# Kernel optimization log

Hardware: AMD Instinct MI355X
Metric: run time of the kernel (lower is better)

Reference implementation:

```python
import jax, jax.numpy as jnp
import numpy as np

HEAD = 8  # number of attention heads (init kwarg)


def setup_inputs() -> dict:
    key = jax.random.key(0)
    k1, k2, k3 = jax.random.split(key, 3)
    b, H, W, c = 8, 32, 32, 512
    dim = 512
    x = jax.random.normal(k1, (b, H, W, c), dtype=jnp.float32)
    # 1x1 Conv == per-pixel matmul over channels
    w_qkv = jax.random.normal(k2, (c, 3 * dim), dtype=jnp.float32) * (c ** -0.5)
    w_out = jax.random.normal(k3, (dim, dim), dtype=jnp.float32) * (dim ** -0.5)
    b_out = jnp.zeros((dim,), dtype=jnp.float32)
    return {"x": x, "w_qkv": w_qkv, "w_out": w_out, "b_out": b_out}


def reference(x, w_qkv, w_out, b_out):
    b, H, W, c = x.shape
    n = H * W
    # QKV 1x1-conv projection (no bias)
    qkv = jnp.einsum('bhwc,cd->bhwd', x, w_qkv)          # (b, H, W, 3*dim)
    qkv = qkv.reshape(b, n, HEAD, -1)                     # (b, n, head, 3*dh)
    q, k, v = jnp.split(qkv, 3, axis=-1)                  # each (b, n, head, dh)
    scale = b ** -0.5  # NOTE: source scales by batch size, reproduced faithfully
    attn = jax.nn.softmax(jnp.einsum('bihd,bjhd->bhij', q, k) * scale, axis=-1)
    out = jnp.einsum('bhij,bjhd->bihd', attn, v)          # (b, n, head, dh)
    out = out.reshape(b, H, W, -1)                        # (b, H, W, dim)
    # output 1x1-conv projection (with bias)
    return jnp.einsum('bhwc,cd->bhwd', out, w_out) + b_out
```

## Files before the change

kernel.cpp:

```cpp
#include <hip/hip_runtime.h>
#include <hip/hip_bf16.h>

typedef __bf16 bf16x8_t __attribute__((ext_vector_type(8)));
typedef float  f32x4_t  __attribute__((ext_vector_type(4)));
typedef short  s16x4_t  __attribute__((ext_vector_type(4)));
typedef short  s16x8_t  __attribute__((ext_vector_type(8)));

#define NTOK   1024
#define CDIM   512
#define QKVDIM 1536
#define NHEAD  8
#define DHEAD  64
#define C1EXP  0.51007088f
#define C2EXP  34.624681f

__device__ __forceinline__ short f2b(float f) {
    __bf16 h = (__bf16)f; short s; __builtin_memcpy(&s, &h, 2); return s;
}

__device__ __forceinline__ void gld16(const short* g, short* l) {
    __builtin_amdgcn_global_load_lds(
        (const __attribute__((address_space(1))) void*)g,
        (__attribute__((address_space(3))) void*)l, 16, 0, 0);
}

__global__ __launch_bounds__(256) void cvt_w(
    const float* __restrict__ wq, const float* __restrict__ wo,
    short* __restrict__ wqbT, short* __restrict__ wobT)
{
    const int b = blockIdx.x;
    const int t = threadIdx.x;
    const int kk = t & 63, grp = t >> 6;
    if (b < 192) {
        const int K0 = (b & 7) * 64, N0 = (b >> 3) * 64;
#pragma unroll
        for (int s = 0; s < 16; ++s) {
            int n = N0 + grp * 16 + s;
            wqbT[(size_t)n * 512 + K0 + kk] = f2b(wq[(size_t)(K0 + kk) * 1536 + n]);
        }
    } else {
        const int b2 = b - 192;
        const int K0 = (b2 & 7) * 64, N0 = (b2 >> 3) * 64;
#pragma unroll
        for (int s = 0; s < 16; ++s) {
            int n = N0 + grp * 16 + s;
            wobT[(size_t)n * 512 + K0 + kk] = f2b(wo[(size_t)(K0 + kk) * 512 + n]);
        }
    }
}

__global__ __launch_bounds__(256) void gemm_qkv(
    const float* __restrict__ X, const short* __restrict__ Bt,
    short* __restrict__ qk, short* __restrict__ vT)
{
    __shared__ __align__(16) short Al[128 * 64];
    __shared__ __align__(16) short Bl[128 * 64];

    const int t = threadIdx.x;
    const int bid = blockIdx.x;
    const int xcd = bid & 7, jpos = bid >> 3;
    const int tm = xcd * 8 + jpos / 12;
    const int tn = jpos % 12;
    const int N0 = tn * 128, M0 = tm * 128;
    const int w = t >> 6, lane = t & 63;
    const int quad = lane >> 4, mr = lane & 15;
    const int wm = (w >> 1) * 64, wn = (w & 1) * 64;

    int srow[4], soff[4];
#pragma unroll
    for (int r = 0; r < 4; ++r) {
        int ci = r * 256 + t;
        srow[r] = ci >> 3;
        soff[r] = (ci & 7) * 8;
    }
    const float* Ag = X  + (size_t)M0 * 512;
    const short* Bg = Bt + (size_t)N0 * 512;

    const int gr8 = lane >> 3, gc8 = (lane & 7) * 8;

    float4 fa[4][2];
#pragma unroll
    for (int r = 0; r < 4; ++r) {
        const float* pa = Ag + (size_t)srow[r] * 512 + soff[r];
        fa[r][0] = *(const float4*)pa;
        fa[r][1] = *(const float4*)(pa + 4);
    }

    f32x4_t acc[4][4];
#pragma unroll
    for (int ms = 0; ms < 4; ++ms)
#pragma unroll
        for (int ns = 0; ns < 4; ++ns) acc[ms][ns] = f32x4_t{0.f,0.f,0.f,0.f};

#pragma unroll 1
    for (int kc = 0; kc < 8; ++kc) {
        __syncthreads();
#pragma unroll
        for (int r = 0; r < 4; ++r) {
            int lds = srow[r] * 64 + (((soff[r] >> 3) ^ (srow[r] & 7)) * 8);
            s16x8_t va;
            va[0] = f2b(fa[r][0].x); va[1] = f2b(fa[r][0].y);
            va[2] = f2b(fa[r][0].z); va[3] = f2b(fa[r][0].w);
            va[4] = f2b(fa[r][1].x); va[5] = f2b(fa[r][1].y);
            va[6] = f2b(fa[r][1].z); va[7] = f2b(fa[r][1].w);
            *(s16x8_t*)(Al + lds) = va;
        }
#pragma unroll
        for (int c = 0; c < 4; ++c) {
            int ch = w * 4 + c;
            gld16(Bg + (size_t)(ch * 8 + gr8) * 512 + kc * 64 + gc8,
                  Bl + ch * 512);
        }
        __syncthreads();

        if (kc < 7) {
            int k0 = (kc + 1) * 64;
#pragma unroll
            for (int r = 0; r < 4; ++r) {
                const float* pa = Ag + (size_t)srow[r] * 512 + k0 + soff[r];
                fa[r][0] = *(const float4*)pa;
                fa[r][1] = *(const float4*)(pa + 4);
            }
        }
#pragma unroll
        for (int kh = 0; kh < 2; ++kh) {
            bf16x8_t af[4], bf[4];
#pragma unroll
            for (int ms = 0; ms < 4; ++ms) {
                int rr = wm + ms * 16 + mr;
                af[ms] = *(const bf16x8_t*)(Al + rr * 64 + (((kh * 4 + quad) ^ (rr & 7)) * 8));
            }
#pragma unroll
            for (int ns = 0; ns < 4; ++ns) {
                int rr = wn + ns * 16 + mr;
                bf[ns] = *(const bf16x8_t*)(Bl + rr * 64 + (kh * 4 + quad) * 8);
            }
#pragma unroll
            for (int ms = 0; ms < 4; ++ms)
#pragma unroll
                for (int ns = 0; ns < 4; ++ns)
                    acc[ms][ns] = __builtin_amdgcn_mfma_f32_16x16x32_bf16(
                        af[ms], bf[ns], acc[ms][ns], 0, 0, 0);
        }
    }

#pragma unroll
    for (int ms = 0; ms < 4; ++ms) {
        int row = M0 + wm + ms * 16 + quad * 4;
        int bb = row >> 10, ti = row & 1023;
#pragma unroll
        for (int ns = 0; ns < 4; ++ns) {
            int c0 = N0 + wn + ns * 16;
            int hh = c0 / 192, r0 = c0 % 192;
            if (r0 < 128) {
                size_t base = (size_t)row * 1024 + hh * 128 + r0 + mr;
#pragma unroll
                for (int i = 0; i < 4; ++i)
                    qk[base + (size_t)i * 1024] = f2b(acc[ms][ns][i]);
            } else {
                s16x4_t v4;
#pragma unroll
                for (int i = 0; i < 4; ++i) v4[i] = f2b(acc[ms][ns][i]);
                *(s16x4_t*)(vT + ((size_t)(bb * 8 + hh) * 64 + (r0 - 128) + mr) * 1024 + ti) = v4;
            }
        }
    }
}

template <int N, bool BIAS, bool OUTF32>
__global__ __launch_bounds__(256) void gemm128(
    const short* __restrict__ A, const short* __restrict__ Bt,
    const float* __restrict__ bias, void* __restrict__ C)
{
    __shared__ __align__(16) short Al[128 * 64];
    __shared__ __align__(16) short Bl[128 * 64];

    constexpr int TNT = N / 128;
    const int t = threadIdx.x;
    const int bid = blockIdx.x;
    const int xcd = bid & 7, jpos = bid >> 3;
    const int tm = xcd * 8 + jpos / TNT;
    const int tn = jpos % TNT;
    const int N0 = tn * 128, M0 = tm * 128;
    const int w = t >> 6, lane = t & 63;
    const int quad = lane >> 4, mr = lane & 15;
    const int wm = (w >> 1) * 64, wn = (w & 1) * 64;

    const short* Ag = A  + (size_t)M0 * 512;
    const short* Bg = Bt + (size_t)N0 * 512;
    const int gr8 = lane >> 3, gc8 = (lane & 7) * 8;

    f32x4_t acc[4][4];
#pragma unroll
    for (int ms = 0; ms < 4; ++ms)
#pragma unroll
        for (int ns = 0; ns < 4; ++ns) acc[ms][ns] = f32x4_t{0.f,0.f,0.f,0.f};

#pragma unroll 1
    for (int kc = 0; kc < 8; ++kc) {
        __syncthreads();
#pragma unroll
        for (int c = 0; c < 4; ++c) {
            int ch = w * 4 + c;
            const size_t roff = (size_t)(ch * 8 + gr8) * 512 + kc * 64 + gc8;
            gld16(Ag + roff, Al + ch * 512);
            gld16(Bg + roff, Bl + ch * 512);
        }
        __syncthreads();

#pragma unroll
        for (int kh = 0; kh < 2; ++kh) {
            bf16x8_t af[4], bf[4];
#pragma unroll
            for (int ms = 0; ms < 4; ++ms) {
                int rr = wm + ms * 16 + mr;
                af[ms] = *(const bf16x8_t*)(Al + rr * 64 + (kh * 4 + quad) * 8);
            }
#pragma unroll
            for (int ns = 0; ns < 4; ++ns) {
                int rr = wn + ns * 16 + mr;
                bf[ns] = *(const bf16x8_t*)(Bl + rr * 64 + (kh * 4 + quad) * 8);
            }
#pragma unroll
            for (int ms = 0; ms < 4; ++ms)
#pragma unroll
                for (int ns = 0; ns < 4; ++ns)
                    acc[ms][ns] = __builtin_amdgcn_mfma_f32_16x16x32_bf16(
                        af[ms], bf[ns], acc[ms][ns], 0, 0, 0);
        }
    }

#pragma unroll
    for (int ms = 0; ms < 4; ++ms) {
        int row = M0 + wm + ms * 16 + quad * 4;
#pragma unroll
        for (int ns = 0; ns < 4; ++ns) {
            int col = N0 + wn + ns * 16 + mr;
            float bz = BIAS ? bias[col] : 0.f;
#pragma unroll
            for (int i = 0; i < 4; ++i) {
                if constexpr (OUTF32)
                    ((float*)C)[(size_t)(row + i) * N + col] = acc[ms][ns][i] + bz;
                else
                    ((short*)C)[(size_t)(row + i) * N + col] = f2b(acc[ms][ns][i]);
            }
        }
    }
}

__global__ __launch_bounds__(512, 2) void attn_st(
    const short* __restrict__ qk, const short* __restrict__ vT,
    short* __restrict__ aout)
{
    __shared__ __align__(16) short Kl[128 * 72];
    __shared__ __align__(16) short Vt[64 * 136];
    __shared__ __align__(16) short Pl[8][32 * 136];

    const int t = threadIdx.x;
    const int g = blockIdx.x;
    const int qt = (g >> 3) & 3;
    const int h = g & 7, b = g >> 5;
    const int w = t >> 6, lane = t & 63;
    const int quad = lane >> 4, mr = lane & 15;

    const size_t qra = (size_t)(b * NTOK + qt * 256 + w * 32 + mr) * 1024 + h * 128;
    const size_t qrb = qra + (size_t)16 * 1024;
    const bf16x8_t qf0a = *(const bf16x8_t*)(qk + qra + quad * 8);
    const bf16x8_t qf1a = *(const bf16x8_t*)(qk + qra + 32 + quad * 8);
    const bf16x8_t qf0b = *(const bf16x8_t*)(qk + qrb + quad * 8);
    const bf16x8_t qf1b = *(const bf16x8_t*)(qk + qrb + 32 + quad * 8);

    s16x8_t ones_s;
#pragma unroll
    for (int e = 0; e < 8; ++e) ones_s[e] = 0x3F80;
    const bf16x8_t onesv = *(const bf16x8_t*)&ones_s;

    f32x4_t L4a = f32x4_t{0.f,0.f,0.f,0.f}, L4b = f32x4_t{0.f,0.f,0.f,0.f};
    f32x4_t Oa[4], Ob[4];
#pragma unroll
    for (int d = 0; d < 4; ++d) {
        Oa[d] = f32x4_t{0.f,0.f,0.f,0.f};
        Ob[d] = f32x4_t{0.f,0.f,0.f,0.f};
    }

    short* Pma = Pl[w];
    short* Pmb = Pma + 16 * 136;

    const int kr0 = t >> 3, kr1 = kr0 + 64;
    const int kc8 = (t & 7) * 8;
    const int vr0 = t >> 4, vr1 = vr0 + 32;
    const int vc8 = (t & 15) * 8;

    const size_t kg = (size_t)(b * NTOK) * 1024 + h * 128 + 64 + kc8;
    const size_t vg = (size_t)(b * 8 + h) * 64 * 1024 + vc8;

    s16x8_t k0r, k1r, v0r, v1r;
    k0r = *(const s16x8_t*)(qk + kg + (size_t)kr0 * 1024);
    k1r = *(const s16x8_t*)(qk + kg + (size_t)kr1 * 1024);
    v0r = *(const s16x8_t*)(vT + vg + (size_t)vr0 * 1024);
    v1r = *(const s16x8_t*)(vT + vg + (size_t)vr1 * 1024);

#pragma unroll 1
    for (int jt = 0; jt < 8; ++jt) {
        *(s16x8_t*)(Kl + kr0 * 72 + kc8)  = k0r;
        *(s16x8_t*)(Kl + kr1 * 72 + kc8)  = k1r;
        *(s16x8_t*)(Vt + vr0 * 136 + vc8) = v0r;
        *(s16x8_t*)(Vt + vr1 * 136 + vc8) = v1r;
        __syncthreads();

        if (jt < 7) {
            int j0n = (jt + 1) * 128;
            k0r = *(const s16x8_t*)(qk + kg + (size_t)(j0n + kr0) * 1024);
            k1r = *(const s16x8_t*)(qk + kg + (size_t)(j0n + kr1) * 1024);
            v0r = *(const s16x8_t*)(vT + vg + (size_t)vr0 * 1024 + j0n);
            v1r = *(const s16x8_t*)(vT + vg + (size_t)vr1 * 1024 + j0n);
        }

#pragma unroll
        for (int jj = 0; jj < 8; ++jj) {
            const short* kb = Kl + (jj * 16 + mr) * 72 + quad * 8;
            const bf16x8_t kf0 = *(const bf16x8_t*)kb;
            const bf16x8_t kf1 = *(const bf16x8_t*)(kb + 32);
            __builtin_amdgcn_s_setprio(1);
            f32x4_t a0a = __builtin_amdgcn_mfma_f32_16x16x32_bf16(
                kf0, qf0a, f32x4_t{0.f,0.f,0.f,0.f}, 0, 0, 0);
            f32x4_t sa = __builtin_amdgcn_mfma_f32_16x16x32_bf16(
                kf1, qf1a, a0a, 0, 0, 0);
            f32x4_t a0b = __builtin_amdgcn_mfma_f32_16x16x32_bf16(
                kf0, qf0b, f32x4_t{0.f,0.f,0.f,0.f}, 0, 0, 0);
            f32x4_t sb = __builtin_amdgcn_mfma_f32_16x16x32_bf16(
                kf1, qf1b, a0b, 0, 0, 0);
            __builtin_amdgcn_s_setprio(0);
            s16x4_t pva, pvb;
#pragma unroll
            for (int r = 0; r < 4; ++r) {
                pva[r] = f2b(__builtin_amdgcn_exp2f(sa[r] * C1EXP - C2EXP));
                pvb[r] = f2b(__builtin_amdgcn_exp2f(sb[r] * C1EXP - C2EXP));
            }
            *(s16x4_t*)(Pma + mr * 136 + jj * 16 + quad * 4) = pva;
            *(s16x4_t*)(Pmb + mr * 136 + jj * 16 + quad * 4) = pvb;
        }

        bf16x8_t paa[4], pab[4];
#pragma unroll
        for (int ks = 0; ks < 4; ++ks) {
            paa[ks] = *(const bf16x8_t*)(Pma + mr * 136 + ks * 32 + quad * 8);
            pab[ks] = *(const bf16x8_t*)(Pmb + mr * 136 + ks * 32 + quad * 8);
        }

        __builtin_amdgcn_s_setprio(1);
#pragma unroll
        for (int ks = 0; ks < 4; ++ks) {
            L4a = __builtin_amdgcn_mfma_f32_16x16x32_bf16(paa[ks], onesv, L4a, 0, 0, 0);
            L4b = __builtin_amdgcn_mfma_f32_16x16x32_bf16(pab[ks], onesv, L4b, 0, 0, 0);
        }
#pragma unroll
        for (int dt = 0; dt < 4; ++dt) {
            const short* vb = Vt + (dt * 16 + mr) * 136 + quad * 8;
#pragma unroll
            for (int ks = 0; ks < 4; ++ks) {
                const bf16x8_t vf = *(const bf16x8_t*)(vb + ks * 32);
                Oa[dt] = __builtin_amdgcn_mfma_f32_16x16x32_bf16(paa[ks], vf, Oa[dt], 0, 0, 0);
                Ob[dt] = __builtin_amdgcn_mfma_f32_16x16x32_bf16(pab[ks], vf, Ob[dt], 0, 0, 0);
            }
        }
        __builtin_amdgcn_s_setprio(0);
        __syncthreads();
    }

#pragma unroll
    for (int dt = 0; dt < 4; ++dt)
#pragma unroll
        for (int i = 0; i < 4; ++i) {
            Pma[(quad * 4 + i) * 136 + dt * 16 + mr] = f2b(Oa[dt][i] * (1.f / L4a[i]));
            Pmb[(quad * 4 + i) * 136 + dt * 16 + mr] = f2b(Ob[dt][i] * (1.f / L4b[i]));
        }
    __syncthreads();

    const int q2 = lane >> 2, h2 = lane & 3;
#pragma unroll
    for (int it = 0; it < 2; ++it) {
        const int row = it * 16 + q2;
        const size_t tok = (size_t)(b * NTOK + qt * 256 + w * 32 + row);
        s16x8_t o0 = *(const s16x8_t*)(Pma + row * 136 + h2 * 16);
        s16x8_t o1 = *(const s16x8_t*)(Pma + row * 136 + h2 * 16 + 8);
        *(s16x8_t*)(aout + tok * CDIM + h * DHEAD + h2 * 16)     = o0;
        *(s16x8_t*)(aout + tok * CDIM + h * DHEAD + h2 * 16 + 8) = o1;
    }
}

extern "C" void kernel_launch(void* const* d_in, const int* in_sizes, int n_in,
                              void* d_out, int out_size, void* d_ws, size_t ws_size,
                              hipStream_t stream)
{
    const float* x     = (const float*)d_in[0];
    const float* w_qkv = (const float*)d_in[1];
    const float* w_out = (const float*)d_in[2];
    const float* b_out = (const float*)d_in[3];
    for (int i = 0; i < n_in; ++i) {
        if      (in_sizes[i] == 4194304) x     = (const float*)d_in[i];
        else if (in_sizes[i] ==  786432) w_qkv = (const float*)d_in[i];
        else if (in_sizes[i] ==  262144) w_out = (const float*)d_in[i];
        else if (in_sizes[i] ==     512) b_out = (const float*)d_in[i];
    }

    short* qk   = (short*)d_ws;
    short* vT   = (short*)((char*)d_ws + (size_t)8192 * 1024 * 2);
    short* aout = (short*)((char*)d_ws + (size_t)8192 * 1024 * 2 + (size_t)64 * 64 * 1024 * 2);
    short* wobT = (short*)((char*)d_ws + (size_t)33 * 1024 * 1024 + (size_t)1664 * 1024);
    short* wqbT = (short*)d_out + (size_t)8192 * 512;

    cvt_w<<<256, 256, 0, stream>>>(w_qkv, w_out, wqbT, wobT);

    gemm_qkv<<<768, 256, 0, stream>>>(x, wqbT, qk, vT);

    attn_st<<<256, 512, 0, stream>>>(qk, vT, aout);

    gemm128<CDIM, true, true>
        <<<(CDIM / 128) * 64, 256, 0, stream>>>(aout, wobT, b_out, d_out);
}
```

Measured before the change: 141.2 us.

## Prefetch B through registers in the QKV GEMM and double-buffer LDS in gemm128

In the QKV projection kernel, the B tile now goes through registers instead of direct global-to-LDS loads. It is prefetched one K-chunk ahead, alongside the A prefetch, and stored into LDS with the same XOR swizzle as A. The swizzle is meant to reduce LDS bank conflicts on the B fragment reads. In gemm128, LDS is double-buffered so the next K-chunk's global_load_lds is issued before computing on the current buffer, overlapping loads with MFMA. This doubles LDS use in gemm128, which may lower occupancy, and relies on the end-of-iteration barrier for the async LDS loads to be complete.

```diff
diff --git a/kernel.cpp b/kernel.cpp
--- a/kernel.cpp
+++ b/kernel.cpp
@@ -76,14 +76,14 @@
     const float* Ag = X  + (size_t)M0 * 512;
     const short* Bg = Bt + (size_t)N0 * 512;
 
-    const int gr8 = lane >> 3, gc8 = (lane & 7) * 8;
-
-    float4 fa[4][2];
+    float4  fa[4][2];
+    s16x8_t br[4];
 #pragma unroll
     for (int r = 0; r < 4; ++r) {
         const float* pa = Ag + (size_t)srow[r] * 512 + soff[r];
         fa[r][0] = *(const float4*)pa;
         fa[r][1] = *(const float4*)(pa + 4);
+        br[r] = *(const s16x8_t*)(Bg + (size_t)srow[r] * 512 + soff[r]);
     }
 
     f32x4_t acc[4][4];
@@ -104,15 +104,9 @@
             va[4] = f2b(fa[r][1].x); va[5] = f2b(fa[r][1].y);
             va[6] = f2b(fa[r][1].z); va[7] = f2b(fa[r][1].w);
             *(s16x8_t*)(Al + lds) = va;
-        }
-#pragma unroll
-        for (int c = 0; c < 4; ++c) {
-            int ch = w * 4 + c;
-            gld16(Bg + (size_t)(ch * 8 + gr8) * 512 + kc * 64 + gc8,
-                  Bl + ch * 512);
+            *(s16x8_t*)(Bl + lds) = br[r];
         }
         __syncthreads();
-
         if (kc < 7) {
             int k0 = (kc + 1) * 64;
 #pragma unroll
@@ -120,6 +114,7 @@
                 const float* pa = Ag + (size_t)srow[r] * 512 + k0 + soff[r];
                 fa[r][0] = *(const float4*)pa;
                 fa[r][1] = *(const float4*)(pa + 4);
+                br[r] = *(const s16x8_t*)(Bg + (size_t)srow[r] * 512 + k0 + soff[r]);
             }
         }
 #pragma unroll
@@ -133,7 +128,7 @@
 #pragma unroll
             for (int ns = 0; ns < 4; ++ns) {
                 int rr = wn + ns * 16 + mr;
-                bf[ns] = *(const bf16x8_t*)(Bl + rr * 64 + (kh * 4 + quad) * 8);
+                bf[ns] = *(const bf16x8_t*)(Bl + rr * 64 + (((kh * 4 + quad) ^ (rr & 7)) * 8));
             }
 #pragma unroll
             for (int ms = 0; ms < 4; ++ms)
@@ -172,8 +167,8 @@
     const short* __restrict__ A, const short* __restrict__ Bt,
     const float* __restrict__ bias, void* __restrict__ C)
 {
-    __shared__ __align__(16) short Al[128 * 64];
-    __shared__ __align__(16) short Bl[128 * 64];
+    __shared__ __align__(16) short Al[2][128 * 64];
+    __shared__ __align__(16) short Bl[2][128 * 64];
 
     constexpr int TNT = N / 128;
     const int t = threadIdx.x;
@@ -196,17 +191,23 @@
 #pragma unroll
         for (int ns = 0; ns < 4; ++ns) acc[ms][ns] = f32x4_t{0.f,0.f,0.f,0.f};
 
-#pragma unroll 1
-    for (int kc = 0; kc < 8; ++kc) {
-        __syncthreads();
+    auto STAGE = [&](int bf, int kc) {
 #pragma unroll
         for (int c = 0; c < 4; ++c) {
             int ch = w * 4 + c;
             const size_t roff = (size_t)(ch * 8 + gr8) * 512 + kc * 64 + gc8;
-            gld16(Ag + roff, Al + ch * 512);
-            gld16(Bg + roff, Bl + ch * 512);
-        }
-        __syncthreads();
+            gld16(Ag + roff, Al[bf] + ch * 512);
+            gld16(Bg + roff, Bl[bf] + ch * 512);
+        }
+    };
+
+    STAGE(0, 0);
+    __syncthreads();
+
+    int cur = 0;
+#pragma unroll 1
+    for (int kc = 0; kc < 8; ++kc) {
+        if (kc < 7) STAGE(cur ^ 1, kc + 1);
 
 #pragma unroll
         for (int kh = 0; kh < 2; ++kh) {
@@ -214,12 +215,12 @@
 #pragma unroll
             for (int ms = 0; ms < 4; ++ms) {
                 int rr = wm + ms * 16 + mr;
-                af[ms] = *(const bf16x8_t*)(Al + rr * 64 + (kh * 4 + quad) * 8);
+                af[ms] = *(const bf16x8_t*)(Al[cur] + rr * 64 + (kh * 4 + quad) * 8);
             }
 #pragma unroll
             for (int ns = 0; ns < 4; ++ns) {
                 int rr = wn + ns * 16 + mr;
-                bf[ns] = *(const bf16x8_t*)(Bl + rr * 64 + (kh * 4 + quad) * 8);
+                bf[ns] = *(const bf16x8_t*)(Bl[cur] + rr * 64 + (kh * 4 + quad) * 8);
             }
 #pragma unroll
             for (int ms = 0; ms < 4; ++ms)
@@ -228,6 +229,8 @@
                     acc[ms][ns] = __builtin_amdgcn_mfma_f32_16x16x32_bf16(
                         af[ms], bf[ns], acc[ms][ns], 0, 0, 0);
         }
+        __syncthreads();
+        cur ^= 1;
     }
 
 #pragma unroll
```

New measurement: 134.4 us. 4.8% less time.
